# Optimization experiments

Measured on AMD Instinct MI355X. Metric: run time of the kernel, lower is better.

## Reference

```python
import jax, jax.numpy as jnp
import numpy as np

N_NODES = 50000


def gcn_conv(x, edge_index, W, b):
    """PyG GCNConv: add self-loops, symmetric deg^-1/2 normalization,
    linear transform, scatter-add aggregation."""
    n = x.shape[0]
    src, dst = edge_index[0], edge_index[1]
    loop = jnp.arange(n, dtype=src.dtype)
    src = jnp.concatenate([src, loop])          # [E+N]
    dst = jnp.concatenate([dst, loop])          # [E+N]
    w = jnp.ones(src.shape[0], dtype=x.dtype)   # edge_weight=None -> ones
    deg = jax.ops.segment_sum(w, dst, num_segments=n)          # [N]
    dinv = jnp.where(deg > 0, jax.lax.rsqrt(deg), 0.0)
    norm = dinv[src] * w * dinv[dst]            # [E+N]
    h = x @ W                                   # [N, out]
    msg = h[src] * norm[:, None]                # [E+N, out] gather + scale
    out = jax.ops.segment_sum(msg, dst, num_segments=n)        # scatter-add
    return out + b


def setup_inputs() -> dict:
    key = jax.random.key(0)
    k1, k2, k3, k4, k5, k6 = jax.random.split(key, 6)
    in_c, hid_c, out_c = 3, 128, 64
    n_edges = 800000
    x = jax.random.normal(k1, (N_NODES, in_c), dtype=jnp.float32)
    edge_index = jax.random.randint(k2, (2, n_edges), 0, N_NODES, dtype=jnp.int64)
    W1 = jax.random.normal(k3, (in_c, hid_c), dtype=jnp.float32) / np.sqrt(in_c)
    b1 = jnp.zeros((hid_c,), dtype=jnp.float32)
    W2 = jax.random.normal(k4, (hid_c, out_c), dtype=jnp.float32) / np.sqrt(hid_c)
    b2 = jnp.zeros((out_c,), dtype=jnp.float32)
    return {"x": x, "edge_index": edge_index, "W1": W1, "b1": b1, "W2": W2, "b2": b2}


def reference(x, edge_index, W1, b1, W2, b2):
    h = gcn_conv(x, edge_index, W1, b1)
    h = jax.nn.relu(h)
    return gcn_conv(h, edge_index, W2, b2)
```

## Files before the change

### kernel.cpp

```cpp
#include <hip/hip_runtime.h>
#include <hip/hip_bf16.h>

#define HID 128
#define OUTC 64
#define INC 3
#define BCAP 64
#define OVF_CAP 8192
#define NT 64
#define NCBMAX 256
#define CAP8K 8192
#define KPT 8
#define EPT 4

static __device__ __forceinline__ unsigned short f2bf(float f) {
    __hip_bfloat16 b = __float2bfloat16(f);
    return *reinterpret_cast<unsigned short*>(&b);
}
static __device__ __forceinline__ float bf2f(unsigned short u) {
    __hip_bfloat16 b = *reinterpret_cast<__hip_bfloat16*>(&u);
    return __bfloat162float(b);
}


__global__ __launch_bounds__(256) void place2_kernel(const int* __restrict__ src,
                                                     const int* __restrict__ dst, int E, int NCB,
                                                     int* __restrict__ cbcur,
                                                     unsigned int* __restrict__ part,
                                                     int* __restrict__ ovf, int* __restrict__ ovf_cnt) {
    __shared__ int lhist[NCBMAX];
    __shared__ int lbase[NCBMAX];
    int t = threadIdx.x;
    int s0 = blockIdx.x * (256 * KPT);
    for (int i = t; i < NCBMAX; i += 256) lhist[i] = 0;
    __syncthreads();

    unsigned pk[KPT];
    int cbv[KPT];
    bool val[KPT];
#pragma unroll
    for (int i = 0; i < KPT; ++i) {
        int e = s0 + t + i * 256;
        val[i] = (e < E);
        if (val[i]) {
            int d = dst[e], s = src[e];
            cbv[i] = d >> 8;
            pk[i] = (unsigned)s | ((unsigned)(d & 255) << 16);
            atomicAdd(&lhist[cbv[i]], 1);
        }
    }
    __syncthreads();
    for (int i = t; i < NCB; i += 256) {
        int c = lhist[i];
        lbase[i] = c ? atomicAdd(&cbcur[i], c) : 0;
        lhist[i] = 0;
    }
    __syncthreads();
#pragma unroll
    for (int i = 0; i < KPT; ++i) {
        if (val[i]) {
            int cb = cbv[i];
            int p = atomicAdd(&lhist[cb], 1);
            int slot = lbase[cb] + p;
            if (slot < CAP8K) {
                part[(size_t)cb * CAP8K + slot] = pk[i];
            } else {
                int o = atomicAdd(ovf_cnt, 1);
                if (o < OVF_CAP) {
                    ovf[2 * o] = (int)(pk[i] & 0xFFFF);
                    ovf[2 * o + 1] = cb * 256 + (int)((pk[i] >> 16) & 0xFF);
                }
            }
        }
    }
}

__global__ __launch_bounds__(256) void bin_kernel(const unsigned int* __restrict__ part,
                                                  const int* __restrict__ cbcur,
                                                  const float* __restrict__ x, int N,
                                                  int* __restrict__ cursor,
                                                  unsigned short* __restrict__ bucket,
                                                  float4* __restrict__ z4,
                                                  int* __restrict__ ovf, int* __restrict__ ovf_cnt) {
    __shared__ int lcnt[256];
    __shared__ unsigned short lbuck[256 * BCAP];
    int cb = blockIdx.x, t = threadIdx.x;
    lcnt[t] = 0;
    __syncthreads();
    int cnt = cbcur[cb];
    cnt = cnt < CAP8K ? cnt : CAP8K;
    size_t start = (size_t)cb * CAP8K;
    for (int i = t; i < cnt; i += 256) {
        unsigned pk = part[start + i];
        int s = pk & 0xFFFF;
        int ln = (pk >> 16) & 0xFF;
        int p = atomicAdd(&lcnt[ln], 1);
        if (p < BCAP) {
            lbuck[ln * BCAP + p] = (unsigned short)s;
        } else {
            int o = atomicAdd(ovf_cnt, 1);
            if (o < OVF_CAP) { ovf[2 * o] = s; ovf[2 * o + 1] = cb * 256 + ln; }
        }
    }
    __syncthreads();
    int d = cb * 256 + t;
    if (d < N) {
        int deg = lcnt[t];
        cursor[d] = deg;
        float dd = rsqrtf((float)(deg + 1));
        z4[d] = make_float4(dd * x[3 * d], dd * x[3 * d + 1], dd * x[3 * d + 2], dd);
    }
    const uint4* lsrc = (const uint4*)lbuck;
    uint4* gdst = (uint4*)(bucket + (size_t)cb * 256 * BCAP);
    for (int i = t; i < (256 * BCAP * 2) / 16; i += 256) gdst[i] = lsrc[i];
}


template <typename IT>
__global__ void fill_bucket_kernel(const int* __restrict__ src, const int* __restrict__ dst, int E,
                                   int T, int* __restrict__ cursor, IT* __restrict__ bucket,
                                   int* __restrict__ ovf, int* __restrict__ ovf_cnt) {
    int tid = blockIdx.x * blockDim.x + threadIdx.x;
    int d[EPT], s[EPT], p[EPT];
    bool v[EPT];
#pragma unroll
    for (int k = 0; k < EPT; ++k) {
        int e = tid + k * T;
        v[k] = (e < E);
        d[k] = v[k] ? dst[e] : 0;
        s[k] = v[k] ? src[e] : 0;
    }
#pragma unroll
    for (int k = 0; k < EPT; ++k)
        if (v[k]) p[k] = atomicAdd(&cursor[d[k]], 1);
#pragma unroll
    for (int k = 0; k < EPT; ++k) {
        if (v[k]) {
            if (p[k] < BCAP) {
                bucket[(size_t)d[k] * BCAP + p[k]] = (IT)s[k];
            } else {
                int o = atomicAdd(ovf_cnt, 1);
                if (o < OVF_CAP) { ovf[2 * o] = s[k]; ovf[2 * o + 1] = d[k]; }
            }
        }
    }
}

__global__ void z4_kernel(const float* __restrict__ x, const int* __restrict__ cursor,
                          float4* __restrict__ z4, int N) {
    int i = blockIdx.x * blockDim.x + threadIdx.x;
    if (i < N) {
        float dd = rsqrtf((float)(cursor[i] + 1));
        z4[i] = make_float4(dd * x[3 * i], dd * x[3 * i + 1], dd * x[3 * i + 2], dd);
    }
}


template <typename IT>
__global__ void gather1_kernel(const int* __restrict__ cursor, const IT* __restrict__ bucket,
                               const float4* __restrict__ z4, float4* __restrict__ agg4, int N) {
    int wid = threadIdx.x >> 6;
    int j = threadIdx.x & 63;
    int d = blockIdx.x * 4 + wid;
    if (d >= N) return;
    int cnt = cursor[d];
    cnt = cnt < BCAP ? cnt : BCAP;
    float a0 = 0.f, a1 = 0.f, a2 = 0.f;
    if (j < cnt) {
        int s = (int)bucket[(size_t)d * BCAP + j];
        float4 zv = z4[s];
        a0 = zv.x; a1 = zv.y; a2 = zv.z;
    }
#pragma unroll
    for (int o = 32; o > 0; o >>= 1) {
        a0 += __shfl_xor(a0, o, 64);
        a1 += __shfl_xor(a1, o, 64);
        a2 += __shfl_xor(a2, o, 64);
    }
    if (j == 0) agg4[d] = make_float4(a0, a1, a2, 0.f);
}

__global__ void ovf1_kernel(const int* __restrict__ ovf, const int* __restrict__ ovf_cnt,
                            const float4* __restrict__ z4, float4* __restrict__ agg4) {
    int cnt = *ovf_cnt;
    cnt = cnt < OVF_CAP ? cnt : OVF_CAP;
    for (int t = threadIdx.x; t < cnt; t += blockDim.x) {
        int s = ovf[2 * t], d = ovf[2 * t + 1];
        float4 zv = z4[s];
        float* a = (float*)&agg4[d];
        atomicAdd(a + 0, zv.x);
        atomicAdd(a + 1, zv.y);
        atomicAdd(a + 2, zv.z);
    }
}


__global__ __launch_bounds__(256) void hidden_kernel(const float4* __restrict__ agg4,
                                                     const float4* __restrict__ z4,
                                                     const float* __restrict__ W1,
                                                     const float* __restrict__ b1,
                                                     const float* __restrict__ W2,
                                                     unsigned short* __restrict__ hs2b, int N) {
    __shared__ float h_s[HID][NT];
    __shared__ float w_s[HID * OUTC];
    int t = threadIdx.x;
    int base = blockIdx.x * NT;

    for (int i = t; i < HID * OUTC; i += 256) w_s[i] = W2[i];

    {
        int n = t & 63;
        int d = base + n;
        float u0 = 0.f, u1 = 0.f, u2 = 0.f;
        if (d < N) {
            float4 zv = z4[d];
            float4 av = agg4[d];
            float dd = zv.w;
            u0 = dd * (av.x + zv.x);
            u1 = dd * (av.y + zv.y);
            u2 = dd * (av.z + zv.z);
        }
        int k0 = t >> 6;
#pragma unroll
        for (int i = 0; i < HID / 4; ++i) {
            int k = k0 + 4 * i;
            float v = u0 * W1[k] + u1 * W1[HID + k] + u2 * W1[2 * HID + k] + b1[k];
            h_s[k][n] = fmaxf(v, 0.f);
        }
    }
    __syncthreads();

    int tx = t & 15, ty = t >> 4;
    float acc[4][4] = {};
#pragma unroll 8
    for (int k = 0; k < HID; ++k) {
        float4 hv = *(const float4*)&h_s[k][ty * 4];
        float4 wv = *(const float4*)&w_s[k * OUTC + tx * 4];
        float hr[4] = {hv.x, hv.y, hv.z, hv.w};
        float wr[4] = {wv.x, wv.y, wv.z, wv.w};
#pragma unroll
        for (int r = 0; r < 4; ++r)
#pragma unroll
            for (int c = 0; c < 4; ++c) acc[r][c] = fmaf(hr[r], wr[c], acc[r][c]);
    }

#pragma unroll
    for (int r = 0; r < 4; ++r) {
        int n = ty * 4 + r;
        int d = base + n;
        if (d < N) {
            float dd = z4[d].w;
            ushort4 o;
            o.x = f2bf(dd * acc[r][0]);
            o.y = f2bf(dd * acc[r][1]);
            o.z = f2bf(dd * acc[r][2]);
            o.w = f2bf(dd * acc[r][3]);
            *(ushort4*)&hs2b[(size_t)d * OUTC + tx * 4] = o;
        }
    }
}


template <typename IT>
__global__ __launch_bounds__(256) void gather2_kernel(const int* __restrict__ cursor,
                                                      const IT* __restrict__ bucket,
                                                      const unsigned int* __restrict__ hs2w,
                                                      const float4* __restrict__ z4,
                                                      const float* __restrict__ b2,
                                                      float* __restrict__ out, int N) {
    __shared__ int slist[8 * BCAP];
    int t = threadIdx.x;
    int base = blockIdx.x * 8;
    int lim = (N - base) * BCAP;
    int total = 8 * BCAP;
    if (lim > total) lim = total;
    for (int i = t; i < lim; i += 256) slist[i] = (int)bucket[(size_t)base * BCAP + i];
    __syncthreads();

    int g = t >> 5;
    int q = t & 31;
    int d = base + g;
    if (d >= N) return;
    int cnt = cursor[d];
    cnt = cnt < BCAP ? cnt : BCAP;
    const int* my = &slist[g * BCAP];
    float ax = 0.f, ay = 0.f;
    int k = 0;
    for (; k + 8 <= cnt; k += 8) {
        unsigned u0 = hs2w[(size_t)my[k]     * 32 + q];
        unsigned u1 = hs2w[(size_t)my[k + 1] * 32 + q];
        unsigned u2 = hs2w[(size_t)my[k + 2] * 32 + q];
        unsigned u3 = hs2w[(size_t)my[k + 3] * 32 + q];
        unsigned u4 = hs2w[(size_t)my[k + 4] * 32 + q];
        unsigned u5 = hs2w[(size_t)my[k + 5] * 32 + q];
        unsigned u6 = hs2w[(size_t)my[k + 6] * 32 + q];
        unsigned u7 = hs2w[(size_t)my[k + 7] * 32 + q];
        ax += ((bf2f(u0 & 0xFFFF) + bf2f(u1 & 0xFFFF)) + (bf2f(u2 & 0xFFFF) + bf2f(u3 & 0xFFFF)))
            + ((bf2f(u4 & 0xFFFF) + bf2f(u5 & 0xFFFF)) + (bf2f(u6 & 0xFFFF) + bf2f(u7 & 0xFFFF)));
        ay += ((bf2f(u0 >> 16) + bf2f(u1 >> 16)) + (bf2f(u2 >> 16) + bf2f(u3 >> 16)))
            + ((bf2f(u4 >> 16) + bf2f(u5 >> 16)) + (bf2f(u6 >> 16) + bf2f(u7 >> 16)));
    }
    for (; k + 4 <= cnt; k += 4) {
        unsigned u0 = hs2w[(size_t)my[k]     * 32 + q];
        unsigned u1 = hs2w[(size_t)my[k + 1] * 32 + q];
        unsigned u2 = hs2w[(size_t)my[k + 2] * 32 + q];
        unsigned u3 = hs2w[(size_t)my[k + 3] * 32 + q];
        ax += (bf2f(u0 & 0xFFFF) + bf2f(u1 & 0xFFFF)) + (bf2f(u2 & 0xFFFF) + bf2f(u3 & 0xFFFF));
        ay += (bf2f(u0 >> 16) + bf2f(u1 >> 16)) + (bf2f(u2 >> 16) + bf2f(u3 >> 16));
    }
    for (; k < cnt; ++k) {
        unsigned u = hs2w[(size_t)my[k] * 32 + q];
        ax += bf2f(u & 0xFFFF);
        ay += bf2f(u >> 16);
    }
    unsigned us = hs2w[(size_t)d * 32 + q];
    float dd = z4[d].w;
    float2 bb = *(const float2*)&b2[2 * q];
    float2 o;
    o.x = dd * (ax + bf2f(us & 0xFFFF)) + bb.x;
    o.y = dd * (ay + bf2f(us >> 16)) + bb.y;
    *(float2*)&out[(size_t)d * OUTC + 2 * q] = o;
}

__global__ void ovf2_kernel(const int* __restrict__ ovf, const int* __restrict__ ovf_cnt,
                            const unsigned short* __restrict__ hs2b, const float4* __restrict__ z4,
                            float* __restrict__ out) {
    int cnt = *ovf_cnt;
    cnt = cnt < OVF_CAP ? cnt : OVF_CAP;
    for (int t = threadIdx.x; t < cnt * OUTC; t += blockDim.x) {
        int o = t >> 6, j = t & 63;
        int s = ovf[2 * o], d = ovf[2 * o + 1];
        atomicAdd(&out[(size_t)d * OUTC + j], z4[d].w * bf2f(hs2b[(size_t)s * OUTC + j]));
    }
}

static inline size_t align256(size_t v) { return (v + 255) & ~(size_t)255; }

extern "C" void kernel_launch(void* const* d_in, const int* in_sizes, int n_in,
                              void* d_out, int out_size, void* d_ws, size_t ws_size,
                              hipStream_t stream) {
    const float* x  = (const float*)d_in[0];
    const int*   ei = (const int*)d_in[1];
    const float* W1 = (const float*)d_in[2];
    const float* b1 = (const float*)d_in[3];
    const float* W2 = (const float*)d_in[4];
    const float* b2 = (const float*)d_in[5];
    float* out = (float*)d_out;

    const int N = in_sizes[0] / INC;
    const int E = in_sizes[1] / 2;
    const int* src = ei;
    const int* dst = ei + E;
    const bool u16 = (N <= 65535);
    const int NCB = (N + 255) >> 8;

    char* ws = (char*)d_ws;
    size_t off = 0;
    int*    cursor  = (int*)(ws + off);    off += align256((size_t)N * 4);
    float4* z4      = (float4*)(ws + off); off += align256((size_t)N * 16);
    float4* agg4    = (float4*)(ws + off); off += align256((size_t)N * 16);
    int*    cbcur   = (int*)(ws + off);    off += (size_t)NCBMAX * 4;
    int*    ovf_cnt = (int*)(ws + off);    off += 256;
    int*    ovf     = (int*)(ws + off);    off += (size_t)OVF_CAP * 8;
    unsigned int* part = (unsigned int*)(ws + off);
    off += align256(u16 ? (size_t)NCB * CAP8K * 4 : 0);
    void*   bucket  = (void*)(ws + off);
    off += align256(u16 ? (size_t)NCB * 256 * BCAP * 2 : (size_t)N * BCAP * 4);
    unsigned short* hs2b = (unsigned short*)(ws + off); off += (size_t)N * OUTC * 2;
    const unsigned int* hs2w = (const unsigned int*)hs2b;

    const int B = 256;

    if (u16) {
        hipMemsetAsync(cbcur, 0, (size_t)NCBMAX * 4 + 256, stream);
        int NB = (E + 256 * KPT - 1) / (256 * KPT);
        place2_kernel<<<NB, B, 0, stream>>>(src, dst, E, NCB, cbcur, part, ovf, ovf_cnt);
        bin_kernel<<<NCB, B, 0, stream>>>(part, cbcur, x, N, cursor,
                                          (unsigned short*)bucket, z4, ovf, ovf_cnt);
    } else {
        hipMemsetAsync(cursor, 0, (size_t)N * sizeof(int), stream);
        hipMemsetAsync(ovf_cnt, 0, 64, stream);
        int grid = (E + B * EPT - 1) / (B * EPT);
        int T = grid * B;
        fill_bucket_kernel<int><<<grid, B, 0, stream>>>(src, dst, E, T, cursor, (int*)bucket,
                                                        ovf, ovf_cnt);
        z4_kernel<<<(N + B - 1) / B, B, 0, stream>>>(x, cursor, z4, N);
    }

    if (u16)
        gather1_kernel<unsigned short><<<(N + 3) / 4, B, 0, stream>>>(
            cursor, (const unsigned short*)bucket, z4, agg4, N);
    else
        gather1_kernel<int><<<(N + 3) / 4, B, 0, stream>>>(
            cursor, (const int*)bucket, z4, agg4, N);
    ovf1_kernel<<<1, B, 0, stream>>>(ovf, ovf_cnt, z4, agg4);

    hidden_kernel<<<(N + NT - 1) / NT, 256, 0, stream>>>(agg4, z4, W1, b1, W2, hs2b, N);

    if (u16)
        gather2_kernel<unsigned short><<<(N + 7) / 8, B, 0, stream>>>(
            cursor, (const unsigned short*)bucket, hs2w, z4, b2, out, N);
    else
        gather2_kernel<int><<<(N + 7) / 8, B, 0, stream>>>(
            cursor, (const int*)bucket, hs2w, z4, b2, out, N);
    ovf2_kernel<<<1, B, 0, stream>>>(ovf, ovf_cnt, hs2b, z4, out);
}
```

Measured before the change: 148.2 us.

## Fold overflow edges into hidden/gather2 kernels and widen gather2 loads to 8 bytes

Removes the two single-block overflow kernels (ovf1, ovf2). Each destination node now scans the overflow list inside hidden_kernel and gather2_kernel, which saves two launches and the atomics. Gather2 also changes from 32 lanes per node with 4-byte loads to 16 lanes per node with 8-byte uint2 loads, handling 16 nodes per block. The risk is that when overflow is non-empty every thread scans the whole list linearly. With a degree cap of 64 and about 16 edges per node on average, overflow should be nearly empty for these inputs.

```diff
diff --git a/kernel.cpp b/kernel.cpp
--- a/kernel.cpp
+++ b/kernel.cpp
@@ -179,27 +179,15 @@
     if (j == 0) agg4[d] = make_float4(a0, a1, a2, 0.f);
 }
 
-__global__ void ovf1_kernel(const int* __restrict__ ovf, const int* __restrict__ ovf_cnt,
-                            const float4* __restrict__ z4, float4* __restrict__ agg4) {
-    int cnt = *ovf_cnt;
-    cnt = cnt < OVF_CAP ? cnt : OVF_CAP;
-    for (int t = threadIdx.x; t < cnt; t += blockDim.x) {
-        int s = ovf[2 * t], d = ovf[2 * t + 1];
-        float4 zv = z4[s];
-        float* a = (float*)&agg4[d];
-        atomicAdd(a + 0, zv.x);
-        atomicAdd(a + 1, zv.y);
-        atomicAdd(a + 2, zv.z);
-    }
-}
-
 
 __global__ __launch_bounds__(256) void hidden_kernel(const float4* __restrict__ agg4,
                                                      const float4* __restrict__ z4,
                                                      const float* __restrict__ W1,
                                                      const float* __restrict__ b1,
                                                      const float* __restrict__ W2,
-                                                     unsigned short* __restrict__ hs2b, int N) {
+                                                     unsigned short* __restrict__ hs2b, int N,
+                                                     const int* __restrict__ ovf,
+                                                     const int* __restrict__ ovf_cnt) {
     __shared__ float h_s[HID][NT];
     __shared__ float w_s[HID * OUTC];
     int t = threadIdx.x;
@@ -218,6 +206,16 @@
             u0 = dd * (av.x + zv.x);
             u1 = dd * (av.y + zv.y);
             u2 = dd * (av.z + zv.z);
+            int oc = *ovf_cnt;
+            if (oc > 0) {
+                oc = oc < OVF_CAP ? oc : OVF_CAP;
+                for (int i = 0; i < oc; ++i) {
+                    if (ovf[2 * i + 1] == d) {
+                        float4 zs = z4[ovf[2 * i]];
+                        u0 += dd * zs.x; u1 += dd * zs.y; u2 += dd * zs.z;
+                    }
+                }
+            }
         }
         int k0 = t >> 6;
 #pragma unroll
@@ -263,74 +261,87 @@
 template <typename IT>
 __global__ __launch_bounds__(256) void gather2_kernel(const int* __restrict__ cursor,
                                                       const IT* __restrict__ bucket,
-                                                      const unsigned int* __restrict__ hs2w,
+                                                      const uint2* __restrict__ hs2v,
                                                       const float4* __restrict__ z4,
                                                       const float* __restrict__ b2,
-                                                      float* __restrict__ out, int N) {
-    __shared__ int slist[8 * BCAP];
+                                                      float* __restrict__ out, int N,
+                                                      const int* __restrict__ ovf,
+                                                      const int* __restrict__ ovf_cnt) {
+    __shared__ int slist[16 * BCAP];
     int t = threadIdx.x;
-    int base = blockIdx.x * 8;
+    int base = blockIdx.x * 16;
     int lim = (N - base) * BCAP;
-    int total = 8 * BCAP;
+    int total = 16 * BCAP;
     if (lim > total) lim = total;
     for (int i = t; i < lim; i += 256) slist[i] = (int)bucket[(size_t)base * BCAP + i];
     __syncthreads();
 
-    int g = t >> 5;
-    int q = t & 31;
+    int g = t >> 4;
+    int q = t & 15;
     int d = base + g;
     if (d >= N) return;
     int cnt = cursor[d];
     cnt = cnt < BCAP ? cnt : BCAP;
     const int* my = &slist[g * BCAP];
-    float ax = 0.f, ay = 0.f;
+    float a0 = 0.f, a1 = 0.f, a2 = 0.f, a3 = 0.f;
     int k = 0;
     for (; k + 8 <= cnt; k += 8) {
-        unsigned u0 = hs2w[(size_t)my[k]     * 32 + q];
-        unsigned u1 = hs2w[(size_t)my[k + 1] * 32 + q];
-        unsigned u2 = hs2w[(size_t)my[k + 2] * 32 + q];
-        unsigned u3 = hs2w[(size_t)my[k + 3] * 32 + q];
-        unsigned u4 = hs2w[(size_t)my[k + 4] * 32 + q];
-        unsigned u5 = hs2w[(size_t)my[k + 5] * 32 + q];
-        unsigned u6 = hs2w[(size_t)my[k + 6] * 32 + q];
-        unsigned u7 = hs2w[(size_t)my[k + 7] * 32 + q];
-        ax += ((bf2f(u0 & 0xFFFF) + bf2f(u1 & 0xFFFF)) + (bf2f(u2 & 0xFFFF) + bf2f(u3 & 0xFFFF)))
-            + ((bf2f(u4 & 0xFFFF) + bf2f(u5 & 0xFFFF)) + (bf2f(u6 & 0xFFFF) + bf2f(u7 & 0xFFFF)));
-        ay += ((bf2f(u0 >> 16) + bf2f(u1 >> 16)) + (bf2f(u2 >> 16) + bf2f(u3 >> 16)))
-            + ((bf2f(u4 >> 16) + bf2f(u5 >> 16)) + (bf2f(u6 >> 16) + bf2f(u7 >> 16)));
+        uint2 u0 = hs2v[(size_t)my[k]     * 16 + q];
+        uint2 u1 = hs2v[(size_t)my[k + 1] * 16 + q];
+        uint2 u2 = hs2v[(size_t)my[k + 2] * 16 + q];
+        uint2 u3 = hs2v[(size_t)my[k + 3] * 16 + q];
+        uint2 u4 = hs2v[(size_t)my[k + 4] * 16 + q];
+        uint2 u5 = hs2v[(size_t)my[k + 5] * 16 + q];
+        uint2 u6 = hs2v[(size_t)my[k + 6] * 16 + q];
+        uint2 u7 = hs2v[(size_t)my[k + 7] * 16 + q];
+        a0 += ((bf2f(u0.x & 0xFFFF) + bf2f(u1.x & 0xFFFF)) + (bf2f(u2.x & 0xFFFF) + bf2f(u3.x & 0xFFFF)))
+            + ((bf2f(u4.x & 0xFFFF) + bf2f(u5.x & 0xFFFF)) + (bf2f(u6.x & 0xFFFF) + bf2f(u7.x & 0xFFFF)));
+        a1 += ((bf2f(u0.x >> 16) + bf2f(u1.x >> 16)) + (bf2f(u2.x >> 16) + bf2f(u3.x >> 16)))
+            + ((bf2f(u4.x >> 16) + bf2f(u5.x >> 16)) + (bf2f(u6.x >> 16) + bf2f(u7.x >> 16)));
+        a2 += ((bf2f(u0.y & 0xFFFF) + bf2f(u1.y & 0xFFFF)) + (bf2f(u2.y & 0xFFFF) + bf2f(u3.y & 0xFFFF)))
+            + ((bf2f(u4.y & 0xFFFF) + bf2f(u5.y & 0xFFFF)) + (bf2f(u6.y & 0xFFFF) + bf2f(u7.y & 0xFFFF)));
+        a3 += ((bf2f(u0.y >> 16) + bf2f(u1.y >> 16)) + (bf2f(u2.y >> 16) + bf2f(u3.y >> 16)))
+            + ((bf2f(u4.y >> 16) + bf2f(u5.y >> 16)) + (bf2f(u6.y >> 16) + bf2f(u7.y >> 16)));
     }
     for (; k + 4 <= cnt; k += 4) {
-        unsigned u0 = hs2w[(size_t)my[k]     * 32 + q];
-        unsigned u1 = hs2w[(size_t)my[k + 1] * 32 + q];
-        unsigned u2 = hs2w[(size_t)my[k + 2] * 32 + q];
-        unsigned u3 = hs2w[(size_t)my[k + 3] * 32 + q];
-        ax += (bf2f(u0 & 0xFFFF) + bf2f(u1 & 0xFFFF)) + (bf2f(u2 & 0xFFFF) + bf2f(u3 & 0xFFFF));
-        ay += (bf2f(u0 >> 16) + bf2f(u1 >> 16)) + (bf2f(u2 >> 16) + bf2f(u3 >> 16));
+        uint2 u0 = hs2v[(size_t)my[k]     * 16 + q];
+        uint2 u1 = hs2v[(size_t)my[k + 1] * 16 + q];
+        uint2 u2 = hs2v[(size_t)my[k + 2] * 16 + q];
+        uint2 u3 = hs2v[(size_t)my[k + 3] * 16 + q];
+        a0 += (bf2f(u0.x & 0xFFFF) + bf2f(u1.x & 0xFFFF)) + (bf2f(u2.x & 0xFFFF) + bf2f(u3.x & 0xFFFF));
+        a1 += (bf2f(u0.x >> 16) + bf2f(u1.x >> 16)) + (bf2f(u2.x >> 16) + bf2f(u3.x >> 16));
+        a2 += (bf2f(u0.y & 0xFFFF) + bf2f(u1.y & 0xFFFF)) + (bf2f(u2.y & 0xFFFF) + bf2f(u3.y & 0xFFFF));
+        a3 += (bf2f(u0.y >> 16) + bf2f(u1.y >> 16)) + (bf2f(u2.y >> 16) + bf2f(u3.y >> 16));
     }
     for (; k < cnt; ++k) {
-        unsigned u = hs2w[(size_t)my[k] * 32 + q];
-        ax += bf2f(u & 0xFFFF);
-        ay += bf2f(u >> 16);
-    }
-    unsigned us = hs2w[(size_t)d * 32 + q];
+        uint2 u = hs2v[(size_t)my[k] * 16 + q];
+        a0 += bf2f(u.x & 0xFFFF);
+        a1 += bf2f(u.x >> 16);
+        a2 += bf2f(u.y & 0xFFFF);
+        a3 += bf2f(u.y >> 16);
+    }
+    int oc = *ovf_cnt;
+    if (oc > 0) {
+        oc = oc < OVF_CAP ? oc : OVF_CAP;
+        for (int i = 0; i < oc; ++i) {
+            if (ovf[2 * i + 1] == d) {
+                uint2 u = hs2v[(size_t)ovf[2 * i] * 16 + q];
+                a0 += bf2f(u.x & 0xFFFF);
+                a1 += bf2f(u.x >> 16);
+                a2 += bf2f(u.y & 0xFFFF);
+                a3 += bf2f(u.y >> 16);
+            }
+        }
+    }
+    uint2 us = hs2v[(size_t)d * 16 + q];
     float dd = z4[d].w;
-    float2 bb = *(const float2*)&b2[2 * q];
-    float2 o;
-    o.x = dd * (ax + bf2f(us & 0xFFFF)) + bb.x;
-    o.y = dd * (ay + bf2f(us >> 16)) + bb.y;
-    *(float2*)&out[(size_t)d * OUTC + 2 * q] = o;
-}
-
-__global__ void ovf2_kernel(const int* __restrict__ ovf, const int* __restrict__ ovf_cnt,
-                            const unsigned short* __restrict__ hs2b, const float4* __restrict__ z4,
-                            float* __restrict__ out) {
-    int cnt = *ovf_cnt;
-    cnt = cnt < OVF_CAP ? cnt : OVF_CAP;
-    for (int t = threadIdx.x; t < cnt * OUTC; t += blockDim.x) {
-        int o = t >> 6, j = t & 63;
-        int s = ovf[2 * o], d = ovf[2 * o + 1];
-        atomicAdd(&out[(size_t)d * OUTC + j], z4[d].w * bf2f(hs2b[(size_t)s * OUTC + j]));
-    }
+    float4 bb = *(const float4*)&b2[4 * q];
+    float4 o;
+    o.x = dd * (a0 + bf2f(us.x & 0xFFFF)) + bb.x;
+    o.y = dd * (a1 + bf2f(us.x >> 16)) + bb.y;
+    o.z = dd * (a2 + bf2f(us.y & 0xFFFF)) + bb.z;
+    o.w = dd * (a3 + bf2f(us.y >> 16)) + bb.w;
+    *(float4*)&out[(size_t)d * OUTC + 4 * q] = o;
 }
 
 static inline size_t align256(size_t v) { return (v + 255) & ~(size_t)255; }
@@ -366,7 +377,7 @@
     void*   bucket  = (void*)(ws + off);
     off += align256(u16 ? (size_t)NCB * 256 * BCAP * 2 : (size_t)N * BCAP * 4);
     unsigned short* hs2b = (unsigned short*)(ws + off); off += (size_t)N * OUTC * 2;
-    const unsigned int* hs2w = (const unsigned int*)hs2b;
+    const uint2* hs2v = (const uint2*)hs2b;
 
     const int B = 256;
 
@@ -392,15 +403,14 @@
     else
         gather1_kernel<int><<<(N + 3) / 4, B, 0, stream>>>(
             cursor, (const int*)bucket, z4, agg4, N);
-    ovf1_kernel<<<1, B, 0, stream>>>(ovf, ovf_cnt, z4, agg4);
-
-    hidden_kernel<<<(N + NT - 1) / NT, 256, 0, stream>>>(agg4, z4, W1, b1, W2, hs2b, N);
+
+    hidden_kernel<<<(N + NT - 1) / NT, 256, 0, stream>>>(agg4, z4, W1, b1, W2, hs2b, N,
+                                                         ovf, ovf_cnt);
 
     if (u16)
-        gather2_kernel<unsigned short><<<(N + 7) / 8, B, 0, stream>>>(
-            cursor, (const unsigned short*)bucket, hs2w, z4, b2, out, N);
+        gather2_kernel<unsigned short><<<(N + 15) / 16, B, 0, stream>>>(
+            cursor, (const unsigned short*)bucket, hs2v, z4, b2, out, N, ovf, ovf_cnt);
     else
-        gather2_kernel<int><<<(N + 7) / 8, B, 0, stream>>>(
-            cursor, (const int*)bucket, hs2w, z4, b2, out, N);
-    ovf2_kernel<<<1, B, 0, stream>>>(ovf, ovf_cnt, hs2b, z4, out);
-}
+        gather2_kernel<int><<<(N + 15) / 16, B, 0, stream>>>(
+            cursor, (const int*)bucket, hs2v, z4, b2, out, N, ovf, ovf_cnt);
+}
```

Result: faster. 143.7 us (-3.1%).
